# Optimization experiments

Hardware: AMD Instinct MI355X
Metric: run time of the kernel (lower is better)

## Reference

```python
import jax, jax.numpy as jnp
import numpy as np

N = 50000
E = 1600000


def _cheb_norm(edge_index, edge_weight, n):
    # ChebConv sym normalization with lambda_max=2: L_hat = -D^{-1/2} A D^{-1/2}
    row, col = edge_index[0], edge_index[1]
    deg = jax.ops.segment_sum(edge_weight, row, num_segments=n)
    disq = jnp.where(deg > 0, jax.lax.rsqrt(jnp.where(deg > 0, deg, 1.0)), 0.0)
    return -edge_weight * disq[row] * disq[col]


def _prop(x, edge_index, norm, n):
    # Tx_1[dst] = sum_e norm_e * x[src_e]
    row, col = edge_index[0], edge_index[1]
    return jax.ops.segment_sum(norm[:, None] * x[row], col, num_segments=n)


def setup_inputs() -> dict:
    key = jax.random.key(0)
    ks = jax.random.split(key, 12)
    edge_index = jax.random.randint(ks[0], (2, E), 0, N, dtype=jnp.int32)
    s = lambda *sh: 1.0 / np.sqrt(sh[-2] if len(sh) > 1 else 1.0)
    return {
        "x": jax.random.normal(ks[1], (N, 32), dtype=jnp.float32),
        "edge_weight": jax.random.uniform(ks[2], (E,), dtype=jnp.float32),
        "Wx0": jax.random.normal(ks[3], (3, 32, 64), dtype=jnp.float32) * (1.0 / np.sqrt(32)),
        "Wx1": jax.random.normal(ks[4], (3, 32, 64), dtype=jnp.float32) * (1.0 / np.sqrt(32)),
        "bx": jax.random.normal(ks[5], (3, 64), dtype=jnp.float32) * 0.02,
        "Wh0": jax.random.normal(ks[6], (3, 64, 64), dtype=jnp.float32) * (1.0 / np.sqrt(64)),
        "Wh1": jax.random.normal(ks[7], (3, 64, 64), dtype=jnp.float32) * (1.0 / np.sqrt(64)),
        "bh": jax.random.normal(ks[8], (3, 64), dtype=jnp.float32) * 0.02,
        "Wlin": jax.random.normal(ks[9], (64, 1), dtype=jnp.float32) * (1.0 / np.sqrt(64)),
        "blin": jax.random.normal(ks[10], (1,), dtype=jnp.float32) * 0.02,
        "edge_index": edge_index,
    }


def reference(x, edge_weight, Wx0, Wx1, bx, Wh0, Wh1, bh, Wlin, blin, edge_index):
    n = x.shape[0]
    norm = _cheb_norm(edge_index, edge_weight, n)

    # Input-side ChebConv (K=2) for the three gates, sharing one propagate.
    Tx = _prop(x, edge_index, norm, n)                       # [N, in]
    gx = jnp.einsum('nf,gfo->gno', x, Wx0) + jnp.einsum('nf,gfo->gno', Tx, Wx1) + bx[:, None, :]

    H = jnp.zeros((n, 64), dtype=x.dtype)
    TH = _prop(H, edge_index, norm, n)
    gh = jnp.einsum('nf,gfo->gno', H, Wh0[:2]) + jnp.einsum('nf,gfo->gno', TH, Wh1[:2]) + bh[:2, None, :]

    Z = jax.nn.sigmoid(gx[0] + gh[0])
    R = jax.nn.sigmoid(gx[1] + gh[1])

    HR = H * R
    THR = _prop(HR, edge_index, norm, n)
    Hh = HR @ Wh0[2] + THR @ Wh1[2] + bh[2]
    Ht = jnp.tanh(gx[2] + Hh)

    H = Z * H + (1.0 - Z) * Ht
    out = H @ Wlin + blin                                    # [N, 1]
    return out.squeeze(-1)
```

## Files before the change

kernel.cpp:

```cpp
#include <hip/hip_runtime.h>

#define T256 256
#define SB 1024
#define BIG 1024
#define SEG 8
#define RANGE_C 25000
#define HALF_C 12500
#define RANGE_D 25000
#define RANGE_B 25000
#define ITEMS 8


__global__ void __launch_bounds__(BIG)
histc_kernel(const int* __restrict__ col, int* __restrict__ H, int E, int N, int chunk) {
  __shared__ unsigned sc32[HALF_C];
  int b = blockIdx.x;
  int lo = blockIdx.y * RANGE_C;
  int hi = min(lo + RANGE_C, N);
  int len = hi - lo;
  long base = (long)b * chunk;
  int cnt = (int)min((long)chunk, (long)E - base);
  if (cnt < 0) cnt = 0;
  int t = threadIdx.x;
  int halfLen = (len + 1) >> 1;
  for (int i = t; i < halfLen; i += BIG) sc32[i] = 0u;
  __syncthreads();
  for (int i = t; i < cnt; i += BIG) {
    int c = col[base + i];
    if (c >= lo && c < hi) {
      int cc = c - lo;
      atomicAdd(&sc32[cc >> 1], 1u << ((cc & 1) << 4));
    }
  }
  __syncthreads();
  for (int i = t; i < len; i += BIG)
    H[(long)b * N + lo + i] = (int)((sc32[i >> 1] >> ((i & 1) << 4)) & 0xFFFFu);
}

__global__ void __launch_bounds__(BIG)
histd_kernel(const int* __restrict__ row, const float* __restrict__ w,
             float* __restrict__ degH, int E, int N, int chunk) {
  __shared__ float sd[RANGE_D];
  int b = blockIdx.x;
  int lo = blockIdx.y * RANGE_D;
  int hi = min(lo + RANGE_D, N);
  int len = hi - lo;
  long base = (long)b * chunk;
  int cnt = (int)min((long)chunk, (long)E - base);
  if (cnt < 0) cnt = 0;
  int t = threadIdx.x;
  for (int i = t; i < len; i += BIG) sd[i] = 0.f;
  __syncthreads();
  for (int i = t; i < cnt; i += BIG) {
    long e = base + i;
    int r = row[e];
    if (r >= lo && r < hi) atomicAdd(&sd[r - lo], w[e]);
  }
  __syncthreads();
  for (int i = t; i < len; i += BIG) degH[(long)b * N + lo + i] = sd[i];
}


__global__ void colseg1_kernel(const int* __restrict__ H, const float* __restrict__ degH,
                               int* __restrict__ segsum, float* __restrict__ segd,
                               int N, int LB) {
  int c = blockIdx.x * blockDim.x + threadIdx.x;
  int s = blockIdx.y;
  if (c >= N) return;
  long base = (long)s * LB * N + c;
  int sum = 0;
  float d = 0.f;
  for (int j = 0; j < LB; j++) {
    sum += H[base + (long)j * N];
    d += degH[base + (long)j * N];
  }
  segsum[(long)s * N + c] = sum;
  segd[(long)s * N + c] = d;
}

__global__ void colseg2_kernel(int* __restrict__ segsum, const float* __restrict__ segd,
                               float* __restrict__ disq, int* __restrict__ starts, int N) {
  int c = blockIdx.x * blockDim.x + threadIdx.x;
  if (c >= N) return;
  int run = 0;
  float d = 0.f;
#pragma unroll
  for (int s = 0; s < SEG; s++) {
    long i = (long)s * N + c;
    int v = segsum[i];
    segsum[i] = run;
    run += v;
    d += segd[i];
  }
  starts[c] = run;
  disq[c] = (d > 0.f) ? rsqrtf(d) : 0.f;
}

__global__ void colseg3_kernel(int* __restrict__ H, const int* __restrict__ segsum,
                               int N, int LB) {
  int c = blockIdx.x * blockDim.x + threadIdx.x;
  int s = blockIdx.y;
  if (c >= N) return;
  int run = segsum[(long)s * N + c];
  long base = (long)s * LB * N + c;
  for (int j = 0; j < LB; j++) {
    long i = base + (long)j * N;
    int h = H[i];
    H[i] = run;
    run += h;
  }
}

__global__ void colscan_kernel(int* __restrict__ H, const float* __restrict__ degH,
                               float* __restrict__ disq, int* __restrict__ cnt,
                               int N, int nB) {
  int c = blockIdx.x * blockDim.x + threadIdx.x;
  if (c >= N) return;
  int s = 0;
  float d = 0.f;
  for (int b = 0; b < nB; b++) {
    long idx = (long)b * N + c;
    int h = H[idx];
    H[idx] = s;
    s += h;
    d += degH[idx];
  }
  cnt[c] = s;
  disq[c] = (d > 0.f) ? rsqrtf(d) : 0.f;
}

__global__ void __launch_bounds__(SB)
scan1_kernel(int* __restrict__ a, int* __restrict__ bsum, int n) {
  __shared__ int s[SB];
  int t = threadIdx.x;
  int g0 = blockIdx.x * (SB * ITEMS) + t * ITEMS;
  int v[ITEMS];
  int tot = 0;
#pragma unroll
  for (int k = 0; k < ITEMS; k++) {
    int g = g0 + k;
    int u = (g < n) ? a[g] : 0;
    v[k] = u; tot += u;
  }
  s[t] = tot;
  __syncthreads();
  for (int d = 1; d < SB; d <<= 1) {
    int u = (t >= d) ? s[t - d] : 0;
    __syncthreads();
    s[t] += u;
    __syncthreads();
  }
  int run = s[t] - tot;
#pragma unroll
  for (int k = 0; k < ITEMS; k++) {
    int g = g0 + k;
    if (g < n) a[g] = run;
    run += v[k];
  }
  if (t == SB - 1) bsum[blockIdx.x] = s[SB - 1];
}

__global__ void __launch_bounds__(SB)
scan_top_kernel(int* __restrict__ bsum, int nb) {
  __shared__ int s[SB];
  int t = threadIdx.x;
  int v = (t < nb) ? bsum[t] : 0;
  s[t] = v;
  __syncthreads();
  for (int d = 1; d < SB; d <<= 1) {
    int u = (t >= d) ? s[t - d] : 0;
    __syncthreads();
    s[t] += u;
    __syncthreads();
  }
  if (t < nb) bsum[t] = s[t] - v;
}

__global__ void scan_add_kernel(int* __restrict__ a, const int* __restrict__ bsum, int n) {
  int g = blockIdx.x * blockDim.x + threadIdx.x;
  if (g < n) a[g] += bsum[g >> 13];
}

__global__ void __launch_bounds__(BIG)
bucket2_kernel(const int* __restrict__ row, const int* __restrict__ col,
               const float* __restrict__ w, const float* __restrict__ disq,
               const int* __restrict__ H, const int* __restrict__ starts,
               int2* __restrict__ pairs, int E, int N, int chunk) {
  __shared__ int cur[RANGE_B];
  int b = blockIdx.x;
  int lo = blockIdx.y * RANGE_B;
  int hi = min(lo + RANGE_B, N);
  int len = hi - lo;
  long base = (long)b * chunk;
  int cnt = (int)min((long)chunk, (long)E - base);
  if (cnt < 0) cnt = 0;
  int t = threadIdx.x;
  for (int i = t; i < len; i += BIG)
    cur[i] = H[(long)b * N + lo + i] + starts[lo + i];
  __syncthreads();
  for (int i = t; i < cnt; i += BIG) {
    long e = base + i;
    int c = col[e];
    if (c >= lo && c < hi) {
      int r = row[e];
      float nm = -w[e] * disq[r] * disq[c];
      int pos = atomicAdd(&cur[c - lo], 1);
      pairs[pos] = make_int2(r, __float_as_int(nm));
    }
  }
}


__global__ void zero_kernel(int* __restrict__ p, long n) {
  long i = (long)blockIdx.x * blockDim.x + threadIdx.x;
  long stride = (long)gridDim.x * blockDim.x;
  for (; i < n; i += stride) p[i] = 0;
}

__global__ void deghist_dev_kernel(const float* __restrict__ w, const int* __restrict__ row,
                                   const int* __restrict__ col, float* __restrict__ deg,
                                   int* __restrict__ cntArr, int E) {
  int e = blockIdx.x * blockDim.x + threadIdx.x;
  if (e < E) {
    atomicAdd(&deg[row[e]], w[e]);
    atomicAdd(&cntArr[col[e]], 1);
  }
}

__global__ void bucket_dev_kernel(const float* __restrict__ w, const int* __restrict__ row,
                                  const int* __restrict__ col, const float* __restrict__ disq,
                                  int* __restrict__ off, int2* __restrict__ pairs, int E) {
  int e = blockIdx.x * blockDim.x + threadIdx.x;
  if (e >= E) return;
  int r = row[e], c = col[e];
  float v = -w[e] * disq[r] * disq[c];
  int p = atomicAdd(&off[c], 1);
  pairs[p] = make_int2(r, __float_as_int(v));
}


template <int MODE>
__global__ void gather_kernel(const float* __restrict__ x, const int* __restrict__ S,
                              const int2* __restrict__ pairs, float* __restrict__ Tx,
                              int n, int E) {
  int wid = (int)(((long)blockIdx.x * blockDim.x + threadIdx.x) >> 6);
  if (wid >= n) return;
  int lane = threadIdx.x & 63;
  int slot = lane >> 3;
  int f4 = lane & 7;
  int start, end;
  if (MODE == 0) { start = S[wid]; end = (wid + 1 < n) ? S[wid + 1] : E; }
  else           { start = wid ? S[wid - 1] : 0; end = S[wid]; }
  float4 acc = make_float4(0.f, 0.f, 0.f, 0.f);
  int i = start + slot;
  for (; i + 8 < end; i += 16) {
    int2 p0 = pairs[i];
    int2 p1 = pairs[i + 8];
    float4 x0 = *(const float4*)(x + (long)p0.x * 32 + f4 * 4);
    float4 x1 = *(const float4*)(x + (long)p1.x * 32 + f4 * 4);
    float v0 = __int_as_float(p0.y);
    float v1 = __int_as_float(p1.y);
    acc.x += v0 * x0.x; acc.y += v0 * x0.y; acc.z += v0 * x0.z; acc.w += v0 * x0.w;
    acc.x += v1 * x1.x; acc.y += v1 * x1.y; acc.z += v1 * x1.z; acc.w += v1 * x1.w;
  }
  if (i < end) {
    int2 p0 = pairs[i];
    float4 x0 = *(const float4*)(x + (long)p0.x * 32 + f4 * 4);
    float v0 = __int_as_float(p0.y);
    acc.x += v0 * x0.x; acc.y += v0 * x0.y; acc.z += v0 * x0.z; acc.w += v0 * x0.w;
  }
#pragma unroll
  for (int d = 8; d < 64; d <<= 1) {
    acc.x += __shfl_xor(acc.x, d);
    acc.y += __shfl_xor(acc.y, d);
    acc.z += __shfl_xor(acc.z, d);
    acc.w += __shfl_xor(acc.w, d);
  }
  if (slot == 0) *(float4*)(Tx + (long)wid * 32 + f4 * 4) = acc;
}

__global__ void __launch_bounds__(T256)
gate_lds_kernel(const float* __restrict__ x, const float* __restrict__ Tx,
                const float* __restrict__ Wx0, const float* __restrict__ Wx1,
                const float* __restrict__ bx, const float* __restrict__ bh,
                const float* __restrict__ Wlin, const float* __restrict__ blin,
                float* __restrict__ out, int n) {
  __shared__ float wT[4][2112];
  __shared__ float sb[3][64];
  int tid = threadIdx.x;
  for (int i = tid; i < 8192; i += T256) {
    int m = i >> 11, rem = i & 2047, f = rem >> 6, k = rem & 63;
    const float* src = (m == 0) ? Wx0 : (m == 1) ? Wx1 : (m == 2) ? (Wx0 + 4096) : (Wx1 + 4096);
    wT[m][k * 33 + f] = src[f * 64 + k];
  }
  if (tid < 64) {
    sb[0][tid] = bx[tid] + bh[tid];
    sb[1][tid] = bx[128 + tid] + bh[128 + tid];
    sb[2][tid] = Wlin[tid];
  }
  __syncthreads();

  int lane = tid & 63;
  int wave = blockIdx.x * (T256 / 64) + (tid >> 6);
  int nwaves = gridDim.x * (T256 / 64);
  float bz = sb[0][lane], bt = sb[1][lane], wl = sb[2][lane], bl = blin[0];
  const float* w0 = &wT[0][lane * 33];
  const float* w1 = &wT[1][lane * 33];
  const float* w2 = &wT[2][lane * 33];
  const float* w3 = &wT[3][lane * 33];

  for (int base = wave * 2; base < n; base += nwaves * 2) {
    int node1 = base + 1;
    bool has1 = node1 < n;
    int n1 = has1 ? node1 : base;
    const float4* xp0 = (const float4*)(x + (long)base * 32);
    const float4* tp0 = (const float4*)(Tx + (long)base * 32);
    const float4* xp1 = (const float4*)(x + (long)n1 * 32);
    const float4* tp1 = (const float4*)(Tx + (long)n1 * 32);
    float az0 = bz, at0 = bt, az1 = bz, at1 = bt;
#pragma unroll
    for (int c = 0; c < 8; c++) {
      float4 xa0 = xp0[c], ta0 = tp0[c], xa1 = xp1[c], ta1 = tp1[c];
      int f = c * 4;
      float a, b2, d, g;
      a = w0[f]; b2 = w1[f]; d = w2[f]; g = w3[f];
      az0 += xa0.x * a + ta0.x * b2;  at0 += xa0.x * d + ta0.x * g;
      az1 += xa1.x * a + ta1.x * b2;  at1 += xa1.x * d + ta1.x * g;
      a = w0[f + 1]; b2 = w1[f + 1]; d = w2[f + 1]; g = w3[f + 1];
      az0 += xa0.y * a + ta0.y * b2;  at0 += xa0.y * d + ta0.y * g;
      az1 += xa1.y * a + ta1.y * b2;  at1 += xa1.y * d + ta1.y * g;
      a = w0[f + 2]; b2 = w1[f + 2]; d = w2[f + 2]; g = w3[f + 2];
      az0 += xa0.z * a + ta0.z * b2;  at0 += xa0.z * d + ta0.z * g;
      az1 += xa1.z * a + ta1.z * b2;  at1 += xa1.z * d + ta1.z * g;
      a = w0[f + 3]; b2 = w1[f + 3]; d = w2[f + 3]; g = w3[f + 3];
      az0 += xa0.w * a + ta0.w * b2;  at0 += xa0.w * d + ta0.w * g;
      az1 += xa1.w * a + ta1.w * b2;  at1 += xa1.w * d + ta1.w * g;
    }
    float c0 = __builtin_amdgcn_rcpf(1.0f + __expf(az0)) *
               (1.0f - 2.0f * __builtin_amdgcn_rcpf(__expf(2.0f * at0) + 1.0f)) * wl;
    float c1 = __builtin_amdgcn_rcpf(1.0f + __expf(az1)) *
               (1.0f - 2.0f * __builtin_amdgcn_rcpf(__expf(2.0f * at1) + 1.0f)) * wl;
#pragma unroll
    for (int d = 1; d < 64; d <<= 1) {
      c0 += __shfl_xor(c0, d);
      c1 += __shfl_xor(c1, d);
    }
    if (lane == 0) {
      out[base] = c0 + bl;
      if (has1) out[node1] = c1 + bl;
    }
  }
}

extern "C" void kernel_launch(void* const* d_in, const int* in_sizes, int n_in,
                              void* d_out, int out_size, void* d_ws, size_t ws_size,
                              hipStream_t stream) {
  const float* x    = (const float*)d_in[0];
  const float* ew   = (const float*)d_in[1];
  const float* Wx0  = (const float*)d_in[2];
  const float* Wx1  = (const float*)d_in[3];
  const float* bx   = (const float*)d_in[4];
  const float* bh   = (const float*)d_in[7];
  const float* Wlin = (const float*)d_in[8];
  const float* blin = (const float*)d_in[9];
  const int*   ei   = (const int*)d_in[10];

  int N = in_sizes[0] / 32;
  int E = in_sizes[1];
  const int* row = ei;
  const int* col = ei + E;
  float* out = (float*)d_out;
  long tthreads = (long)N * 64;
  int nRC = (N + RANGE_C - 1) / RANGE_C;
  int nRD = (N + RANGE_D - 1) / RANGE_D;
  int nRB = (N + RANGE_B - 1) / RANGE_B;

  int nBopts[3] = {128, 96, 64};
  int nB = 0;
  size_t wTx = (size_t)N * 32;
  for (int k = 0; k < 3; k++) {
    size_t cb = (size_t)nBopts[k];
    if ((size_t)(E + nBopts[k] - 1) / nBopts[k] > 65535) continue;
    size_t h = cb * N;
    size_t region = h > (size_t)2 * E ? h : (size_t)2 * E;
    size_t tot = wTx + N + N + 1024 + h + region;
    if (tot * 4 <= ws_size) { nB = nBopts[k]; break; }
  }

  if (nB > 0) {
    float* Tx     = (float*)d_ws;
    int*   segsum = (int*)Tx;
    float* segd   = (float*)(segsum + (size_t)SEG * N);
    float* disq   = Tx + wTx;
    int*   starts = (int*)(disq + N);
    int*   bsum   = starts + N;
    int*   H      = bsum + 1024;
    float* degH   = (float*)(H + (size_t)nB * N);
    int2*  pairs  = (int2*)degH;

    int chunk = (E + nB - 1) / nB;
    int LB = nB / SEG;
    int nb1 = (N + SB * ITEMS - 1) / (SB * ITEMS);
    int cblocks = (N + T256 - 1) / T256;

    histc_kernel<<<dim3(nB, nRC), BIG, 0, stream>>>(col, H, E, N, chunk);
    histd_kernel<<<dim3(nB, nRD), BIG, 0, stream>>>(row, ew, degH, E, N, chunk);
    colseg1_kernel<<<dim3(cblocks, SEG), T256, 0, stream>>>(H, degH, segsum, segd, N, LB);
    colseg2_kernel<<<cblocks, T256, 0, stream>>>(segsum, segd, disq, starts, N);
    colseg3_kernel<<<dim3(cblocks, SEG), T256, 0, stream>>>(H, segsum, N, LB);
    scan1_kernel<<<nb1, SB, 0, stream>>>(starts, bsum, N);
    scan_top_kernel<<<1, SB, 0, stream>>>(bsum, nb1);
    scan_add_kernel<<<cblocks, T256, 0, stream>>>(starts, bsum, N);
    bucket2_kernel<<<dim3(nB, nRB), BIG, 0, stream>>>(row, col, ew, disq, H, starts, pairs, E, N, chunk);
    gather_kernel<0><<<(int)((tthreads + T256 - 1) / T256), T256, 0, stream>>>(
        x, starts, pairs, Tx, N, E);
    gate_lds_kernel<<<1024, T256, 0, stream>>>(x, Tx, Wx0, Wx1, bx, bh, Wlin, blin, out, N);
  } else {
    float* Tx     = (float*)d_ws;
    float* disq   = Tx + wTx;
    int*   starts = (int*)(disq + N);
    int*   bsum   = starts + N;
    int*   H      = bsum + 1024;
    float* degH   = (float*)(H + N);
    size_t head = wTx + N + N + 1024 + N + N;
    if (head & 1) head++;
    int2* pairs = (int2*)((float*)d_ws + head);
    int nb1 = (N + SB * ITEMS - 1) / (SB * ITEMS);
    int eb = (E + T256 - 1) / T256;

    zero_kernel<<<256, T256, 0, stream>>>(H, N);
    zero_kernel<<<256, T256, 0, stream>>>((int*)degH, N);
    deghist_dev_kernel<<<eb, T256, 0, stream>>>(ew, row, col, degH, H, E);
    colscan_kernel<<<(N + T256 - 1) / T256, T256, 0, stream>>>(H, degH, disq, starts, N, 1);
    scan1_kernel<<<nb1, SB, 0, stream>>>(starts, bsum, N);
    scan_top_kernel<<<1, SB, 0, stream>>>(bsum, nb1);
    scan_add_kernel<<<(N + T256 - 1) / T256, T256, 0, stream>>>(starts, bsum, N);
    bucket_dev_kernel<<<eb, T256, 0, stream>>>(ew, row, col, disq, starts, pairs, E);
    gather_kernel<1><<<(int)((tthreads + T256 - 1) / T256), T256, 0, stream>>>(
        x, starts, pairs, Tx, N, E);
    gate_lds_kernel<<<1024, T256, 0, stream>>>(x, Tx, Wx0, Wx1, bx, bh, Wlin, blin, out, N);
  }
}
```

Measured before the change: 155.2 us.

## Fuse count and degree histograms and retile edge chunks to smaller node ranges

Merges the column-count and row-degree histogram kernels into one pass that reads row, col and weight together. The edge split drops from 128/96/64 chunks to a fixed 32, and the node range per block shrinks from 25000 to 6250, so each block holds a smaller LDS histogram and more blocks run at once. Fewer chunks also shrink the per-chunk histogram arrays that the column-segment reductions must sum. The cost is that each edge is now read by 8 range blocks instead of 2, and with chunk = E/32 = 50000 the 16-bit packed counters could overflow if one node drew very many edges in a chunk.

```diff
diff --git a/kernel.cpp b/kernel.cpp
--- a/kernel.cpp
+++ b/kernel.cpp
@@ -3,20 +3,22 @@
 #define T256 256
 #define SB 1024
 #define BIG 1024
+#define NB 32
 #define SEG 8
-#define RANGE_C 25000
-#define HALF_C 12500
-#define RANGE_D 25000
-#define RANGE_B 25000
+#define RANGE 6250
+#define HALF_R 3125
 #define ITEMS 8
 
 
 __global__ void __launch_bounds__(BIG)
-histc_kernel(const int* __restrict__ col, int* __restrict__ H, int E, int N, int chunk) {
-  __shared__ unsigned sc32[HALF_C];
+histcd_kernel(const int* __restrict__ row, const int* __restrict__ col,
+              const float* __restrict__ w, int* __restrict__ H,
+              float* __restrict__ degH, int E, int N, int chunk) {
+  __shared__ unsigned sc32[HALF_R];
+  __shared__ float sd[RANGE];
   int b = blockIdx.x;
-  int lo = blockIdx.y * RANGE_C;
-  int hi = min(lo + RANGE_C, N);
+  int lo = blockIdx.y * RANGE;
+  int hi = min(lo + RANGE, N);
   int len = hi - lo;
   long base = (long)b * chunk;
   int cnt = (int)min((long)chunk, (long)E - base);
@@ -24,40 +26,23 @@
   int t = threadIdx.x;
   int halfLen = (len + 1) >> 1;
   for (int i = t; i < halfLen; i += BIG) sc32[i] = 0u;
+  for (int i = t; i < len; i += BIG) sd[i] = 0.f;
   __syncthreads();
   for (int i = t; i < cnt; i += BIG) {
-    int c = col[base + i];
+    long e = base + i;
+    int c = col[e];
+    int r = row[e];
     if (c >= lo && c < hi) {
       int cc = c - lo;
       atomicAdd(&sc32[cc >> 1], 1u << ((cc & 1) << 4));
     }
-  }
-  __syncthreads();
-  for (int i = t; i < len; i += BIG)
+    if (r >= lo && r < hi) atomicAdd(&sd[r - lo], w[e]);
+  }
+  __syncthreads();
+  for (int i = t; i < len; i += BIG) {
     H[(long)b * N + lo + i] = (int)((sc32[i >> 1] >> ((i & 1) << 4)) & 0xFFFFu);
-}
-
-__global__ void __launch_bounds__(BIG)
-histd_kernel(const int* __restrict__ row, const float* __restrict__ w,
-             float* __restrict__ degH, int E, int N, int chunk) {
-  __shared__ float sd[RANGE_D];
-  int b = blockIdx.x;
-  int lo = blockIdx.y * RANGE_D;
-  int hi = min(lo + RANGE_D, N);
-  int len = hi - lo;
-  long base = (long)b * chunk;
-  int cnt = (int)min((long)chunk, (long)E - base);
-  if (cnt < 0) cnt = 0;
-  int t = threadIdx.x;
-  for (int i = t; i < len; i += BIG) sd[i] = 0.f;
-  __syncthreads();
-  for (int i = t; i < cnt; i += BIG) {
-    long e = base + i;
-    int r = row[e];
-    if (r >= lo && r < hi) atomicAdd(&sd[r - lo], w[e]);
-  }
-  __syncthreads();
-  for (int i = t; i < len; i += BIG) degH[(long)b * N + lo + i] = sd[i];
+    degH[(long)b * N + lo + i] = sd[i];
+  }
 }
 
 
@@ -186,10 +171,10 @@
                const float* __restrict__ w, const float* __restrict__ disq,
                const int* __restrict__ H, const int* __restrict__ starts,
                int2* __restrict__ pairs, int E, int N, int chunk) {
-  __shared__ int cur[RANGE_B];
+  __shared__ int cur[RANGE];
   int b = blockIdx.x;
-  int lo = blockIdx.y * RANGE_B;
-  int hi = min(lo + RANGE_B, N);
+  int lo = blockIdx.y * RANGE;
+  int hi = min(lo + RANGE, N);
   int len = hi - lo;
   long base = (long)b * chunk;
   int cnt = (int)min((long)chunk, (long)E - base);
@@ -371,23 +356,16 @@
   const int* col = ei + E;
   float* out = (float*)d_out;
   long tthreads = (long)N * 64;
-  int nRC = (N + RANGE_C - 1) / RANGE_C;
-  int nRD = (N + RANGE_D - 1) / RANGE_D;
-  int nRB = (N + RANGE_B - 1) / RANGE_B;
-
-  int nBopts[3] = {128, 96, 64};
-  int nB = 0;
+  int nR = (N + RANGE - 1) / RANGE;
+  int chunk = (E + NB - 1) / NB;
+
   size_t wTx = (size_t)N * 32;
-  for (int k = 0; k < 3; k++) {
-    size_t cb = (size_t)nBopts[k];
-    if ((size_t)(E + nBopts[k] - 1) / nBopts[k] > 65535) continue;
-    size_t h = cb * N;
-    size_t region = h > (size_t)2 * E ? h : (size_t)2 * E;
-    size_t tot = wTx + N + N + 1024 + h + region;
-    if (tot * 4 <= ws_size) { nB = nBopts[k]; break; }
-  }
-
-  if (nB > 0) {
+  size_t h = (size_t)NB * N;
+  size_t region = h > (size_t)2 * E ? h : (size_t)2 * E;
+  size_t tot = wTx + N + N + 1024 + h + region;
+  bool fits = (tot * 4 <= ws_size) && (chunk <= 65535);
+
+  if (fits) {
     float* Tx     = (float*)d_ws;
     int*   segsum = (int*)Tx;
     float* segd   = (float*)(segsum + (size_t)SEG * N);
@@ -395,23 +373,21 @@
     int*   starts = (int*)(disq + N);
     int*   bsum   = starts + N;
     int*   H      = bsum + 1024;
-    float* degH   = (float*)(H + (size_t)nB * N);
+    float* degH   = (float*)(H + h);
     int2*  pairs  = (int2*)degH;
 
-    int chunk = (E + nB - 1) / nB;
-    int LB = nB / SEG;
+    int LB = NB / SEG;
     int nb1 = (N + SB * ITEMS - 1) / (SB * ITEMS);
     int cblocks = (N + T256 - 1) / T256;
 
-    histc_kernel<<<dim3(nB, nRC), BIG, 0, stream>>>(col, H, E, N, chunk);
-    histd_kernel<<<dim3(nB, nRD), BIG, 0, stream>>>(row, ew, degH, E, N, chunk);
+    histcd_kernel<<<dim3(NB, nR), BIG, 0, stream>>>(row, col, ew, H, degH, E, N, chunk);
     colseg1_kernel<<<dim3(cblocks, SEG), T256, 0, stream>>>(H, degH, segsum, segd, N, LB);
     colseg2_kernel<<<cblocks, T256, 0, stream>>>(segsum, segd, disq, starts, N);
     colseg3_kernel<<<dim3(cblocks, SEG), T256, 0, stream>>>(H, segsum, N, LB);
     scan1_kernel<<<nb1, SB, 0, stream>>>(starts, bsum, N);
     scan_top_kernel<<<1, SB, 0, stream>>>(bsum, nb1);
     scan_add_kernel<<<cblocks, T256, 0, stream>>>(starts, bsum, N);
-    bucket2_kernel<<<dim3(nB, nRB), BIG, 0, stream>>>(row, col, ew, disq, H, starts, pairs, E, N, chunk);
+    bucket2_kernel<<<dim3(NB, nR), BIG, 0, stream>>>(row, col, ew, disq, H, starts, pairs, E, N, chunk);
     gather_kernel<0><<<(int)((tthreads + T256 - 1) / T256), T256, 0, stream>>>(
         x, starts, pairs, Tx, N, E);
     gate_lds_kernel<<<1024, T256, 0, stream>>>(x, Tx, Wx0, Wx1, bx, bh, Wlin, blin, out, N);
```

Result: slower. 166.0 us (+7.0%).

## Fuse column exclusive scan into colseg kernels, dropping separate scan passes

Applied to the files above, without the earlier changes.

Folds the block-local prefix scan of per-column totals into the colseg2 kernel, then adds the global offset directly inside colseg3, so the per-(bucket,column) offsets in H become absolute. This removes scan1 and scan_add launches and the starts add in bucket2. The gather kernel now reads H (first row equals absolute column starts) instead of the starts array. The aim is fewer launches and passes over N-sized arrays in a launch-bound pipeline.

```diff
diff --git a/kernel.cpp b/kernel.cpp
--- a/kernel.cpp
+++ b/kernel.cpp
@@ -59,7 +59,6 @@
   __syncthreads();
   for (int i = t; i < len; i += BIG) degH[(long)b * N + lo + i] = sd[i];
 }
-
 
 __global__ void colseg1_kernel(const int* __restrict__ H, const float* __restrict__ degH,
                                int* __restrict__ segsum, float* __restrict__ segd,
@@ -78,36 +77,115 @@
   segd[(long)s * N + c] = d;
 }
 
-__global__ void colseg2_kernel(int* __restrict__ segsum, const float* __restrict__ segd,
-                               float* __restrict__ disq, int* __restrict__ starts, int N) {
-  int c = blockIdx.x * blockDim.x + threadIdx.x;
-  if (c >= N) return;
+__global__ void __launch_bounds__(T256)
+colseg2b_kernel(int* __restrict__ segsum, const float* __restrict__ segd,
+                float* __restrict__ disq, int* __restrict__ startsLoc,
+                int* __restrict__ bsum, int N) {
+  __shared__ int sc[T256];
+  int t = threadIdx.x;
+  int c = blockIdx.x * T256 + t;
   int run = 0;
   float d = 0.f;
-#pragma unroll
-  for (int s = 0; s < SEG; s++) {
-    long i = (long)s * N + c;
-    int v = segsum[i];
-    segsum[i] = run;
-    run += v;
-    d += segd[i];
-  }
-  starts[c] = run;
-  disq[c] = (d > 0.f) ? rsqrtf(d) : 0.f;
-}
-
-__global__ void colseg3_kernel(int* __restrict__ H, const int* __restrict__ segsum,
-                               int N, int LB) {
+  if (c < N) {
+#pragma unroll
+    for (int s = 0; s < SEG; s++) {
+      long i = (long)s * N + c;
+      int v = segsum[i];
+      segsum[i] = run;
+      run += v;
+      d += segd[i];
+    }
+  }
+  sc[t] = run;
+  __syncthreads();
+  for (int dd = 1; dd < T256; dd <<= 1) {
+    int u = (t >= dd) ? sc[t - dd] : 0;
+    __syncthreads();
+    sc[t] += u;
+    __syncthreads();
+  }
+  if (c < N) {
+    startsLoc[c] = sc[t] - run;
+    disq[c] = (d > 0.f) ? rsqrtf(d) : 0.f;
+  }
+  if (t == T256 - 1) bsum[blockIdx.x] = sc[t];
+}
+
+__global__ void __launch_bounds__(SB)
+scan_top_kernel(int* __restrict__ bsum, int nb) {
+  __shared__ int s[SB];
+  int t = threadIdx.x;
+  int v = (t < nb) ? bsum[t] : 0;
+  s[t] = v;
+  __syncthreads();
+  for (int d = 1; d < SB; d <<= 1) {
+    int u = (t >= d) ? s[t - d] : 0;
+    __syncthreads();
+    s[t] += u;
+    __syncthreads();
+  }
+  if (t < nb) bsum[t] = s[t] - v;
+}
+
+__global__ void colseg3b_kernel(int* __restrict__ H, const int* __restrict__ segsum,
+                                const int* __restrict__ startsLoc, const int* __restrict__ bsum,
+                                int N, int LB) {
   int c = blockIdx.x * blockDim.x + threadIdx.x;
   int s = blockIdx.y;
   if (c >= N) return;
-  int run = segsum[(long)s * N + c];
+  int run = segsum[(long)s * N + c] + startsLoc[c] + bsum[c >> 8];
   long base = (long)s * LB * N + c;
   for (int j = 0; j < LB; j++) {
     long i = base + (long)j * N;
     int h = H[i];
     H[i] = run;
     run += h;
+  }
+}
+
+__global__ void __launch_bounds__(BIG)
+bucket2_kernel(const int* __restrict__ row, const int* __restrict__ col,
+               const float* __restrict__ w, const float* __restrict__ disq,
+               const int* __restrict__ H, int2* __restrict__ pairs,
+               int E, int N, int chunk) {
+  __shared__ int cur[RANGE_B];
+  int b = blockIdx.x;
+  int lo = blockIdx.y * RANGE_B;
+  int hi = min(lo + RANGE_B, N);
+  int len = hi - lo;
+  long base = (long)b * chunk;
+  int cnt = (int)min((long)chunk, (long)E - base);
+  if (cnt < 0) cnt = 0;
+  int t = threadIdx.x;
+  for (int i = t; i < len; i += BIG)
+    cur[i] = H[(long)b * N + lo + i];
+  __syncthreads();
+  for (int i = t; i < cnt; i += BIG) {
+    long e = base + i;
+    int c = col[e];
+    if (c >= lo && c < hi) {
+      int r = row[e];
+      float nm = -w[e] * disq[r] * disq[c];
+      int pos = atomicAdd(&cur[c - lo], 1);
+      pairs[pos] = make_int2(r, __float_as_int(nm));
+    }
+  }
+}
+
+
+__global__ void zero_kernel(int* __restrict__ p, long n) {
+  long i = (long)blockIdx.x * blockDim.x + threadIdx.x;
+  long stride = (long)gridDim.x * blockDim.x;
+  for (; i < n; i += stride) p[i] = 0;
+}
+
+__global__ void deghist_dev_kernel(const float* __restrict__ w, const int* __restrict__ row,
+                                   const int* __restrict__ col, float* __restrict__ deg,
+                                   int* __restrict__ cntArr, int E) {
+  int e = blockIdx.x * blockDim.x + threadIdx.x;
+  if (e < E) {
+    atomicAdd(&deg[row[e]], w[e]);
+    atomicAdd(&cntArr[col[e]], 1);
   }
 }
 
@@ -160,71 +238,9 @@
   if (t == SB - 1) bsum[blockIdx.x] = s[SB - 1];
 }
 
-__global__ void __launch_bounds__(SB)
-scan_top_kernel(int* __restrict__ bsum, int nb) {
-  __shared__ int s[SB];
-  int t = threadIdx.x;
-  int v = (t < nb) ? bsum[t] : 0;
-  s[t] = v;
-  __syncthreads();
-  for (int d = 1; d < SB; d <<= 1) {
-    int u = (t >= d) ? s[t - d] : 0;
-    __syncthreads();
-    s[t] += u;
-    __syncthreads();
-  }
-  if (t < nb) bsum[t] = s[t] - v;
-}
-
 __global__ void scan_add_kernel(int* __restrict__ a, const int* __restrict__ bsum, int n) {
   int g = blockIdx.x * blockDim.x + threadIdx.x;
   if (g < n) a[g] += bsum[g >> 13];
-}
-
-__global__ void __launch_bounds__(BIG)
-bucket2_kernel(const int* __restrict__ row, const int* __restrict__ col,
-               const float* __restrict__ w, const float* __restrict__ disq,
-               const int* __restrict__ H, const int* __restrict__ starts,
-               int2* __restrict__ pairs, int E, int N, int chunk) {
-  __shared__ int cur[RANGE_B];
-  int b = blockIdx.x;
-  int lo = blockIdx.y * RANGE_B;
-  int hi = min(lo + RANGE_B, N);
-  int len = hi - lo;
-  long base = (long)b * chunk;
-  int cnt = (int)min((long)chunk, (long)E - base);
-  if (cnt < 0) cnt = 0;
-  int t = threadIdx.x;
-  for (int i = t; i < len; i += BIG)
-    cur[i] = H[(long)b * N + lo + i] + starts[lo + i];
-  __syncthreads();
-  for (int i = t; i < cnt; i += BIG) {
-    long e = base + i;
-    int c = col[e];
-    if (c >= lo && c < hi) {
-      int r = row[e];
-      float nm = -w[e] * disq[r] * disq[c];
-      int pos = atomicAdd(&cur[c - lo], 1);
-      pairs[pos] = make_int2(r, __float_as_int(nm));
-    }
-  }
-}
-
-
-__global__ void zero_kernel(int* __restrict__ p, long n) {
-  long i = (long)blockIdx.x * blockDim.x + threadIdx.x;
-  long stride = (long)gridDim.x * blockDim.x;
-  for (; i < n; i += stride) p[i] = 0;
-}
-
-__global__ void deghist_dev_kernel(const float* __restrict__ w, const int* __restrict__ row,
-                                   const int* __restrict__ col, float* __restrict__ deg,
-                                   int* __restrict__ cntArr, int E) {
-  int e = blockIdx.x * blockDim.x + threadIdx.x;
-  if (e < E) {
-    atomicAdd(&deg[row[e]], w[e]);
-    atomicAdd(&cntArr[col[e]], 1);
-  }
 }
 
 __global__ void bucket_dev_kernel(const float* __restrict__ w, const int* __restrict__ row,
@@ -392,28 +408,25 @@
     int*   segsum = (int*)Tx;
     float* segd   = (float*)(segsum + (size_t)SEG * N);
     float* disq   = Tx + wTx;
-    int*   starts = (int*)(disq + N);
-    int*   bsum   = starts + N;
+    int*   startsLoc = (int*)(disq + N);
+    int*   bsum   = startsLoc + N;
     int*   H      = bsum + 1024;
     float* degH   = (float*)(H + (size_t)nB * N);
     int2*  pairs  = (int2*)degH;
 
     int chunk = (E + nB - 1) / nB;
     int LB = nB / SEG;
-    int nb1 = (N + SB * ITEMS - 1) / (SB * ITEMS);
     int cblocks = (N + T256 - 1) / T256;
 
     histc_kernel<<<dim3(nB, nRC), BIG, 0, stream>>>(col, H, E, N, chunk);
     histd_kernel<<<dim3(nB, nRD), BIG, 0, stream>>>(row, ew, degH, E, N, chunk);
     colseg1_kernel<<<dim3(cblocks, SEG), T256, 0, stream>>>(H, degH, segsum, segd, N, LB);
-    colseg2_kernel<<<cblocks, T256, 0, stream>>>(segsum, segd, disq, starts, N);
-    colseg3_kernel<<<dim3(cblocks, SEG), T256, 0, stream>>>(H, segsum, N, LB);
-    scan1_kernel<<<nb1, SB, 0, stream>>>(starts, bsum, N);
-    scan_top_kernel<<<1, SB, 0, stream>>>(bsum, nb1);
-    scan_add_kernel<<<cblocks, T256, 0, stream>>>(starts, bsum, N);
-    bucket2_kernel<<<dim3(nB, nRB), BIG, 0, stream>>>(row, col, ew, disq, H, starts, pairs, E, N, chunk);
+    colseg2b_kernel<<<cblocks, T256, 0, stream>>>(segsum, segd, disq, startsLoc, bsum, N);
+    scan_top_kernel<<<1, SB, 0, stream>>>(bsum, cblocks);
+    colseg3b_kernel<<<dim3(cblocks, SEG), T256, 0, stream>>>(H, segsum, startsLoc, bsum, N, LB);
+    bucket2_kernel<<<dim3(nB, nRB), BIG, 0, stream>>>(row, col, ew, disq, H, pairs, E, N, chunk);
     gather_kernel<0><<<(int)((tthreads + T256 - 1) / T256), T256, 0, stream>>>(
-        x, starts, pairs, Tx, N, E);
+        x, H, pairs, Tx, N, E);
     gate_lds_kernel<<<1024, T256, 0, stream>>>(x, Tx, Wx0, Wx1, bx, bh, Wlin, blin, out, N);
   } else {
     float* Tx     = (float*)d_ws;
```

After: 144.3 us. 1.08x faster.
